# Optimization experiments

Hardware: AMD Instinct MI355X
Metric: run time of the kernel (lower is better)

Reference implementation:

```python
import jax, jax.numpy as jnp
import numpy as np

D_MODEL = 768
NUM_HEADS = 8
HEAD_DIM = D_MODEL // NUM_HEADS


def setup_inputs() -> dict:
    key = jax.random.key(0)
    ks = jax.random.split(key, 5)
    B, N = 4, 2048
    scale = 1.0 / np.sqrt(D_MODEL)
    return {
        "x": jax.random.normal(ks[0], (B, N, D_MODEL), dtype=jnp.float32),
        "W_qkv": jax.random.normal(ks[1], (D_MODEL, 3 * D_MODEL), dtype=jnp.float32) * scale,
        "b_qkv": jax.random.normal(ks[2], (3 * D_MODEL,), dtype=jnp.float32) * 0.01,
        "W_out": jax.random.normal(ks[3], (D_MODEL, D_MODEL), dtype=jnp.float32) * scale,
        "b_out": jax.random.normal(ks[4], (D_MODEL,), dtype=jnp.float32) * 0.01,
    }


def reference(x, W_qkv, b_qkv, W_out, b_out):
    B, N, _ = x.shape
    H, Dh = NUM_HEADS, HEAD_DIM
    # fused QKV projection: [B,N,3*D] -> [3,B,H,N,Dh]
    qkv = (x @ W_qkv + b_qkv).reshape(B, N, 3, H, Dh).transpose(2, 0, 3, 1, 4)
    q, k, v = qkv[0], qkv[1], qkv[2]
    # full NxN attention, as in the original (no masking)
    scores = jnp.einsum("bhnd,bhmd->bhnm", q, k) / jnp.sqrt(jnp.float32(Dh)).astype(x.dtype)
    weights = jax.nn.softmax(scores, axis=-1)
    out = jnp.einsum("bhnm,bhmd->bhnd", weights, v)  # [B,H,N,Dh]
    out = out.transpose(0, 2, 1, 3).reshape(B, N, H * Dh)
    return out @ W_out + b_out
```

## Files before the change

kernel.cpp:

```cpp
#include <hip/hip_runtime.h>
#include <hip/hip_bf16.h>
#include <math.h>

#define BB      4
#define NN      2048
#define DM      768
#define NH      8
#define DHH     96
#define BH      (BB*NH)
#define MROWS   (BB*NN)
#define NC_QKV  (3*DM)

typedef short v4s  __attribute__((ext_vector_type(4)));
typedef short v8s  __attribute__((ext_vector_type(8)));
typedef float v4f  __attribute__((ext_vector_type(4)));
typedef float v16f __attribute__((ext_vector_type(16)));
typedef unsigned int u32;

#define SCQ 0.14724599350930152f

static __device__ __forceinline__ ushort f2bf(float f) {
    __hip_bfloat16 h = __float2bfloat16(f);
    return *reinterpret_cast<ushort*>(&h);
}

static __device__ __forceinline__ void gload_lds16(const ushort* g, ushort* l) {
    __builtin_amdgcn_global_load_lds(
        (const __attribute__((address_space(1))) void*)g,
        (__attribute__((address_space(3))) void*)l, 16, 0, 0);
}

static __device__ __forceinline__ v8s load2x4_o16(const ushort* p) {
    union { v4s h[2]; v8s s; } x;
    x.h[0] = *reinterpret_cast<const v4s*>(p);
    x.h[1] = *reinterpret_cast<const v4s*>(p + 16);
    return x.s;
}

static __device__ __forceinline__ v8s pack4(u32 a, u32 b, u32 c, u32 d) {
    union { u32 u[4]; v8s s; } x;
    x.u[0] = a; x.u[1] = b; x.u[2] = c; x.u[3] = d;
    return x.s;
}
static __device__ __forceinline__ u32 bfpair(float lo, float hi) {
    return (u32)f2bf(lo) | ((u32)f2bf(hi) << 16);
}

#define CONV_NB   (MROWS * DM / 8 / 256)
#define CONVT_NB  ((DM / 32) * ((NC_QKV + DM) / 32))

__global__ __launch_bounds__(256)
void prologue_kernel(const float* __restrict__ x, ushort* __restrict__ xbf,
                     const float* __restrict__ Wq, ushort* __restrict__ Wqt,
                     const float* __restrict__ Wo, ushort* __restrict__ Wot)
{
    __shared__ ushort t[32][33];
    const int bid = blockIdx.x;

    if (bid < CONV_NB) {
        const int i = bid * 256 + threadIdx.x;
        const float4* p = reinterpret_cast<const float4*>(x) + (size_t)i * 2;
        float4 a = p[0], b = p[1];
        ushort r[8] = {f2bf(a.x), f2bf(a.y), f2bf(a.z), f2bf(a.w),
                       f2bf(b.x), f2bf(b.y), f2bf(b.z), f2bf(b.w)};
        *reinterpret_cast<v8s*>(xbf + (size_t)i * 8) = *reinterpret_cast<v8s*>(r);
        return;
    }

    const int bid2 = bid - CONV_NB;
    const int kb = bid2 % (DM / 32);
    const int nb = bid2 / (DM / 32);
    const int K = DM;
    const bool isQ = (nb < NC_QKV / 32);
    const float*  W  = isQ ? Wq  : Wo;
    ushort*       Wt = isQ ? Wqt : Wot;
    const int N  = isQ ? NC_QKV : DM;
    const int k0 = kb * 32;
    const int n0 = (isQ ? nb : nb - NC_QKV / 32) * 32;
    const int tx = threadIdx.x & 31, ty = threadIdx.x >> 5;
    #pragma unroll
    for (int r = ty; r < 32; r += 8)
        t[tx][r] = f2bf(W[(size_t)(k0 + r) * N + n0 + tx]);
    __syncthreads();
    #pragma unroll
    for (int r = ty; r < 32; r += 8)
        Wt[(size_t)(n0 + r) * K + k0 + tx] = t[r][tx];
}

template<int SCATTER>
__global__ __launch_bounds__(256)
void gemm_mfma(const ushort* __restrict__ A, const ushort* __restrict__ Bt,
               const float* __restrict__ bias, void* __restrict__ outp,
               int K, int Ncols)
{
    __shared__ ushort As[2][8192];
    __shared__ ushort Bs[2][8192];

    const int tid  = threadIdx.x;
    const int lane = tid & 63;
    const int wv   = tid >> 6;
    const int l31  = lane & 31;
    const int lhi  = lane >> 5;
    const int wr   = wv >> 1, wc = wv & 1;

    const int ny   = gridDim.y;
    const int id   = blockIdx.y * gridDim.x + blockIdx.x;
    const int c8   = id & 7;
    const int j    = id >> 3;
    const int hy   = (j >= (ny >> 1) * 8) ? 1 : 0;
    const int w    = j - hy * (ny >> 1) * 8;
    const int bx   = c8 * 8 + (w & 7);
    const int by   = hy * (ny >> 1) + (w >> 3);
    const int row0 = bx * 128;
    const int col0 = by * 128;

    v16f acc[2][2];
    #pragma unroll
    for (int mi = 0; mi < 2; ++mi)
        #pragma unroll
        for (int nj = 0; nj < 2; ++nj)
            #pragma unroll
            for (int i = 0; i < 16; ++i) acc[mi][nj][i] = 0.0f;

#define STAGE_G(bsel, kk) do {                                                  \
    _Pragma("unroll")                                                           \
    for (int c = 0; c < 4; ++c) {                                               \
        const int g   = c * 4 + wv;                                             \
        const int idx = g * 64 + lane;                                          \
        const int ss  = idx >> 7, rr = idx & 127;                               \
        gload_lds16(&A [(size_t)(row0 + rr) * K + (kk) + ss * 8],               \
                    &As[bsel][g * 512]);                                        \
        gload_lds16(&Bt[(size_t)(col0 + rr) * K + (kk) + ss * 8],               \
                    &Bs[bsel][g * 512]);                                        \
    }                                                                           \
} while (0)

    STAGE_G(0, 0);
    __syncthreads();

    const int nk = K >> 6;
    for (int t = 0; t < nk; ++t) {
        const int cur = t & 1;
        if (t + 1 < nk) STAGE_G(cur ^ 1, (t + 1) << 6);

        #pragma unroll
        for (int s16 = 0; s16 < 4; ++s16) {
            const int ks = s16 * 2 + lhi;
            v8s a0 = *reinterpret_cast<const v8s*>(&As[cur][(size_t)(ks * 128 + 64 * wr + l31) * 8]);
            v8s a1 = *reinterpret_cast<const v8s*>(&As[cur][(size_t)(ks * 128 + 64 * wr + 32 + l31) * 8]);
            v8s b0 = *reinterpret_cast<const v8s*>(&Bs[cur][(size_t)(ks * 128 + 64 * wc + l31) * 8]);
            v8s b1 = *reinterpret_cast<const v8s*>(&Bs[cur][(size_t)(ks * 128 + 64 * wc + 32 + l31) * 8]);
            acc[0][0] = __builtin_amdgcn_mfma_f32_32x32x16_bf16(a0, b0, acc[0][0], 0, 0, 0);
            acc[0][1] = __builtin_amdgcn_mfma_f32_32x32x16_bf16(a0, b1, acc[0][1], 0, 0, 0);
            acc[1][0] = __builtin_amdgcn_mfma_f32_32x32x16_bf16(a1, b0, acc[1][0], 0, 0, 0);
            acc[1][1] = __builtin_amdgcn_mfma_f32_32x32x16_bf16(a1, b1, acc[1][1], 0, 0, 0);
        }
        __syncthreads();
    }
#undef STAGE_G

    #pragma unroll
    for (int nj = 0; nj < 2; ++nj) {
        const int c = col0 + 64 * wc + 32 * nj + l31;
        const float bv = bias[c];
        #pragma unroll
        for (int mi = 0; mi < 2; ++mi) {
            #pragma unroll
            for (int r = 0; r < 16; ++r) {
                const int m = row0 + 64 * wr + 32 * mi + (r & 3) + 8 * (r >> 2) + 4 * lhi;
                float v = acc[mi][nj][r] + bv;
                if (SCATTER) {
                    const int s   = c / DM;
                    const int rem = c - s * DM;
                    const int h   = rem / DHH;
                    const int d   = rem - h * DHH;
                    const int b   = m >> 11;
                    const int n   = m & (NN - 1);
                    if (s == 0) v *= SCQ;
                    ((ushort*)outp)[((size_t)(s * BH + b * NH + h) * NN + n) * DHH + d] = f2bf(v);
                } else {
                    ((float*)outp)[(size_t)m * Ncols + c] = v;
                }
            }
        }
    }
}

__global__ __launch_bounds__(256, 2)
void attn_mfma(const ushort* __restrict__ qkv, ushort* __restrict__ attnout)
{
    __shared__ ushort Ks[6144];
    __shared__ ushort Vt[96][68];

    const int tid  = threadIdx.x;
    const int lane = tid & 63;
    const int wv   = tid >> 6;
    const int l15  = lane & 15;
    const int g4   = lane >> 4;

    const int id   = blockIdx.y * gridDim.x + blockIdx.x;
    const int c8   = id & 7;
    const int j    = id >> 3;
    const int bh   = c8 * 4 + (j & 3);
    const int qblk = j >> 2;
    const int q0   = qblk * 128;
    const int b    = bh >> 3, h = bh & 7;

    const ushort* Qg = qkv + (size_t)bh * NN * DHH;
    const ushort* Kg = qkv + ((size_t)BH + bh) * NN * DHH;
    const ushort* Vg = qkv + ((size_t)2 * BH + bh) * NN * DHH;

    v8s qf[2][3];
    #pragma unroll
    for (int qt = 0; qt < 2; ++qt)
        #pragma unroll
        for (int c = 0; c < 3; ++c)
            qf[qt][c] = *reinterpret_cast<const v8s*>(
                &Qg[(size_t)(q0 + wv * 32 + qt * 16 + l15) * DHH + c * 32 + g4 * 8]);

    v4f o[2][6];
    #pragma unroll
    for (int qt = 0; qt < 2; ++qt)
        #pragma unroll
        for (int dt = 0; dt < 6; ++dt)
            #pragma unroll
            for (int i = 0; i < 4; ++i) o[qt][dt][i] = 0.0f;
    float ds[2] = {0.0f, 0.0f};

    {
        const size_t rowb = (size_t)lane * DHH;
        v8s kr[3], vr[3];
        #pragma unroll
        for (int i = 0; i < 3; ++i) {
            kr[i] = *reinterpret_cast<const v8s*>(&Kg[rowb + (wv * 3 + i) * 8]);
            vr[i] = *reinterpret_cast<const v8s*>(&Vg[rowb + (i * 4 + wv) * 8]);
        }
        #pragma unroll
        for (int i = 0; i < 3; ++i) {
            *reinterpret_cast<v8s*>(&Ks[(wv * 3 + i) * 512 + lane * 8]) = kr[i];
            #pragma unroll
            for (int jj = 0; jj < 8; ++jj)
                Vt[(i * 4 + wv) * 8 + jj][lane] = (ushort)vr[i][jj];
        }
    }
    __syncthreads();

    for (int t = 0; t < 32; ++t) {
        v8s kr0, kr1, kr2, vr0, vr1, vr2;
        if (t < 31) {
            const size_t rowb = (size_t)((t + 1) * 64 + lane) * DHH;
            kr0 = *reinterpret_cast<const v8s*>(&Kg[rowb + (wv * 3 + 0) * 8]);
            kr1 = *reinterpret_cast<const v8s*>(&Kg[rowb + (wv * 3 + 1) * 8]);
            kr2 = *reinterpret_cast<const v8s*>(&Kg[rowb + (wv * 3 + 2) * 8]);
            vr0 = *reinterpret_cast<const v8s*>(&Vg[rowb + (0 * 4 + wv) * 8]);
            vr1 = *reinterpret_cast<const v8s*>(&Vg[rowb + (1 * 4 + wv) * 8]);
            vr2 = *reinterpret_cast<const v8s*>(&Vg[rowb + (2 * 4 + wv) * 8]);
        }

        #pragma unroll
        for (int th = 0; th < 2; ++th) {
            v4f s00, s01, s10, s11;
            #pragma unroll
            for (int i = 0; i < 4; ++i) {
                s00[i] = 0.0f; s01[i] = 0.0f; s10[i] = 0.0f; s11[i] = 0.0f;
            }
            __builtin_amdgcn_s_setprio(1);
            #pragma unroll
            for (int c = 0; c < 3; ++c) {
                v8s kf0 = *reinterpret_cast<const v8s*>(
                    &Ks[((c * 4 + g4) * 64 + (th * 2 + 0) * 16 + l15) * 8]);
                v8s kf1 = *reinterpret_cast<const v8s*>(
                    &Ks[((c * 4 + g4) * 64 + (th * 2 + 1) * 16 + l15) * 8]);
                s00 = __builtin_amdgcn_mfma_f32_16x16x32_bf16(kf0, qf[0][c], s00, 0, 0, 0);
                s01 = __builtin_amdgcn_mfma_f32_16x16x32_bf16(kf1, qf[0][c], s01, 0, 0, 0);
                s10 = __builtin_amdgcn_mfma_f32_16x16x32_bf16(kf0, qf[1][c], s10, 0, 0, 0);
                s11 = __builtin_amdgcn_mfma_f32_16x16x32_bf16(kf1, qf[1][c], s11, 0, 0, 0);
            }
            __builtin_amdgcn_s_setprio(0);

            v8s pf[2];
            #pragma unroll
            for (int qt = 0; qt < 2; ++qt) {
                const v4f& sa = qt ? s10 : s00;
                const v4f& sb = qt ? s11 : s01;
                float e0[4], e1[4];
                #pragma unroll
                for (int r = 0; r < 4; ++r) {
                    e0[r] = exp2f(sa[r]);
                    e1[r] = exp2f(sb[r]);
                    ds[qt] += e0[r] + e1[r];
                }
                pf[qt] = pack4(bfpair(e0[0], e0[1]), bfpair(e0[2], e0[3]),
                               bfpair(e1[0], e1[1]), bfpair(e1[2], e1[3]));
            }

            __builtin_amdgcn_s_setprio(1);
            #pragma unroll
            for (int dt = 0; dt < 6; ++dt) {
                const ushort* vp = &Vt[dt * 16 + l15][th * 32 + g4 * 4];
                v8s va = load2x4_o16(vp);
                o[0][dt] = __builtin_amdgcn_mfma_f32_16x16x32_bf16(va, pf[0], o[0][dt], 0, 0, 0);
                o[1][dt] = __builtin_amdgcn_mfma_f32_16x16x32_bf16(va, pf[1], o[1][dt], 0, 0, 0);
            }
            __builtin_amdgcn_s_setprio(0);
        }

        if (t < 31) {
            __syncthreads();
            *reinterpret_cast<v8s*>(&Ks[(wv * 3 + 0) * 512 + lane * 8]) = kr0;
            *reinterpret_cast<v8s*>(&Ks[(wv * 3 + 1) * 512 + lane * 8]) = kr1;
            *reinterpret_cast<v8s*>(&Ks[(wv * 3 + 2) * 512 + lane * 8]) = kr2;
            #pragma unroll
            for (int jj = 0; jj < 8; ++jj) Vt[(0 * 4 + wv) * 8 + jj][lane] = (ushort)vr0[jj];
            #pragma unroll
            for (int jj = 0; jj < 8; ++jj) Vt[(1 * 4 + wv) * 8 + jj][lane] = (ushort)vr1[jj];
            #pragma unroll
            for (int jj = 0; jj < 8; ++jj) Vt[(2 * 4 + wv) * 8 + jj][lane] = (ushort)vr2[jj];
            __syncthreads();
        }
    }

    #pragma unroll
    for (int qt = 0; qt < 2; ++qt) {
        float d = ds[qt];
        d += __shfl_xor(d, 16, 64);
        d += __shfl_xor(d, 32, 64);
        const float inv = 1.0f / d;
        const int n = q0 + wv * 32 + qt * 16 + l15;
        ushort* orow = attnout + ((size_t)(b * NN + n)) * DM + h * DHH;
        #pragma unroll
        for (int dt = 0; dt < 6; ++dt) {
            const int d0 = dt * 16 + g4 * 4;
            uint2 pk;
            pk.x = bfpair(o[qt][dt][0] * inv, o[qt][dt][1] * inv);
            pk.y = bfpair(o[qt][dt][2] * inv, o[qt][dt][3] * inv);
            *reinterpret_cast<uint2*>(&orow[d0]) = pk;
        }
    }
}

extern "C" void kernel_launch(void* const* d_in, const int* in_sizes, int n_in,
                              void* d_out, int out_size, void* d_ws, size_t ws_size,
                              hipStream_t stream)
{
    (void)in_sizes; (void)n_in; (void)out_size; (void)ws_size;
    const float* x    = (const float*)d_in[0];
    const float* Wqkv = (const float*)d_in[1];
    const float* bqkv = (const float*)d_in[2];
    const float* Wout = (const float*)d_in[3];
    const float* bout = (const float*)d_in[4];
    float* out = (float*)d_out;

    ushort* qkv   = (ushort*)d_ws;
    ushort* ao    = qkv   + (size_t)3 * BH * NN * DHH;
    ushort* xbf   = ao    + (size_t)MROWS * DM;
    ushort* wqkvt = xbf   + (size_t)MROWS * DM;
    ushort* woutt = wqkvt + (size_t)DM * NC_QKV;

    dim3 blk(256);

    prologue_kernel<<<dim3(CONV_NB + CONVT_NB), blk, 0, stream>>>(
        x, xbf, Wqkv, wqkvt, Wout, woutt);

    gemm_mfma<1><<<dim3(MROWS / 128, NC_QKV / 128), blk, 0, stream>>>(
        xbf, wqkvt, bqkv, (void*)qkv, DM, NC_QKV);

    attn_mfma<<<dim3(16, 32), blk, 0, stream>>>(qkv, ao);

    gemm_mfma<0><<<dim3(MROWS / 128, DM / 128), blk, 0, stream>>>(
        ao, woutt, bout, (void*)out, DM, DM);
}
```

Before: 200.5 us.

## Enlarge GEMM tiles to 256x256 with 8 waves and explicit vmcnt pipelining

```diff
diff --git a/kernel.cpp b/kernel.cpp
--- a/kernel.cpp
+++ b/kernel.cpp
@@ -88,35 +88,34 @@
 }
 
 template<int SCATTER>
-__global__ __launch_bounds__(256)
+__global__ __launch_bounds__(512)
 void gemm_mfma(const ushort* __restrict__ A, const ushort* __restrict__ Bt,
                const float* __restrict__ bias, void* __restrict__ outp,
                int K, int Ncols)
 {
-    __shared__ ushort As[2][8192];
-    __shared__ ushort Bs[2][8192];
+    __shared__ ushort As[2][16384];
+    __shared__ ushort Bs[2][16384];
 
     const int tid  = threadIdx.x;
     const int lane = tid & 63;
     const int wv   = tid >> 6;
     const int l31  = lane & 31;
     const int lhi  = lane >> 5;
-    const int wr   = wv >> 1, wc = wv & 1;
-
-    const int ny   = gridDim.y;
-    const int id   = blockIdx.y * gridDim.x + blockIdx.x;
-    const int c8   = id & 7;
-    const int j    = id >> 3;
-    const int hy   = (j >= (ny >> 1) * 8) ? 1 : 0;
-    const int w    = j - hy * (ny >> 1) * 8;
-    const int bx   = c8 * 8 + (w & 7);
-    const int by   = hy * (ny >> 1) + (w >> 3);
-    const int row0 = bx * 128;
-    const int col0 = by * 128;
-
-    v16f acc[2][2];
-    #pragma unroll
-    for (int mi = 0; mi < 2; ++mi)
+    const int wr   = wv >> 2;
+    const int wc   = wv & 3;
+
+    const int nwg = gridDim.x * gridDim.y;
+    const int id  = blockIdx.y * gridDim.x + blockIdx.x;
+    const int cpx = nwg >> 3;
+    const int wg  = (id & 7) * cpx + (id >> 3);
+    const int bx  = wg % gridDim.x;
+    const int by  = wg / gridDim.x;
+    const int row0 = bx * 256;
+    const int col0 = by * 256;
+
+    v16f acc[4][2];
+    #pragma unroll
+    for (int mi = 0; mi < 4; ++mi)
         #pragma unroll
         for (int nj = 0; nj < 2; ++nj)
             #pragma unroll
@@ -124,50 +123,72 @@
 
 #define STAGE_G(bsel, kk) do {                                                  \
     _Pragma("unroll")                                                           \
-    for (int c = 0; c < 4; ++c) {                                               \
-        const int g   = c * 4 + wv;                                             \
-        const int idx = g * 64 + lane;                                          \
-        const int ss  = idx >> 7, rr = idx & 127;                               \
-        gload_lds16(&A [(size_t)(row0 + rr) * K + (kk) + ss * 8],               \
-                    &As[bsel][g * 512]);                                        \
-        gload_lds16(&Bt[(size_t)(col0 + rr) * K + (kk) + ss * 8],               \
-                    &Bs[bsel][g * 512]);                                        \
+    for (int r_ = 0; r_ < 4; ++r_) {                                            \
+        const int idx_ = r_ * 512 + tid;                           \
+        const int ss_  = idx_ >> 8;                             \
+        const int rr_  = idx_ & 255;                            \
+        gload_lds16(&A [(size_t)(row0 + rr_) * K + (kk) + ss_ * 8],             \
+                    &As[bsel][(size_t)idx_ * 8]);                               \
+        gload_lds16(&Bt[(size_t)(col0 + rr_) * K + (kk) + ss_ * 8],             \
+                    &Bs[bsel][(size_t)idx_ * 8]);                               \
     }                                                                           \
 } while (0)
 
+#define FENCE() __builtin_amdgcn_sched_barrier(0)
+#define BARRIER() do { FENCE(); asm volatile("s_barrier" ::: "memory"); FENCE(); } while (0)
+
     STAGE_G(0, 0);
-    __syncthreads();
 
     const int nk = K >> 6;
     for (int t = 0; t < nk; ++t) {
         const int cur = t & 1;
-        if (t + 1 < nk) STAGE_G(cur ^ 1, (t + 1) << 6);
+
+        BARRIER();
+        if (t + 1 < nk) {
+            STAGE_G(cur ^ 1, (t + 1) << 6);
+            FENCE();
+            asm volatile("s_waitcnt vmcnt(8)" ::: "memory");
+            FENCE();
+        } else {
+            FENCE();
+            asm volatile("s_waitcnt vmcnt(0)" ::: "memory");
+            FENCE();
+        }
+        BARRIER();
 
         #pragma unroll
         for (int s16 = 0; s16 < 4; ++s16) {
             const int ks = s16 * 2 + lhi;
-            v8s a0 = *reinterpret_cast<const v8s*>(&As[cur][(size_t)(ks * 128 + 64 * wr + l31) * 8]);
-            v8s a1 = *reinterpret_cast<const v8s*>(&As[cur][(size_t)(ks * 128 + 64 * wr + 32 + l31) * 8]);
-            v8s b0 = *reinterpret_cast<const v8s*>(&Bs[cur][(size_t)(ks * 128 + 64 * wc + l31) * 8]);
-            v8s b1 = *reinterpret_cast<const v8s*>(&Bs[cur][(size_t)(ks * 128 + 64 * wc + 32 + l31) * 8]);
-            acc[0][0] = __builtin_amdgcn_mfma_f32_32x32x16_bf16(a0, b0, acc[0][0], 0, 0, 0);
-            acc[0][1] = __builtin_amdgcn_mfma_f32_32x32x16_bf16(a0, b1, acc[0][1], 0, 0, 0);
-            acc[1][0] = __builtin_amdgcn_mfma_f32_32x32x16_bf16(a1, b0, acc[1][0], 0, 0, 0);
-            acc[1][1] = __builtin_amdgcn_mfma_f32_32x32x16_bf16(a1, b1, acc[1][1], 0, 0, 0);
-        }
-        __syncthreads();
+            v8s a_[4], b_[2];
+            #pragma unroll
+            for (int mi = 0; mi < 4; ++mi)
+                a_[mi] = *reinterpret_cast<const v8s*>(
+                    &As[cur][(size_t)(ks * 256 + wr * 128 + mi * 32 + l31) * 8]);
+            #pragma unroll
+            for (int nj = 0; nj < 2; ++nj)
+                b_[nj] = *reinterpret_cast<const v8s*>(
+                    &Bs[cur][(size_t)(ks * 256 + wc * 64 + nj * 32 + l31) * 8]);
+            #pragma unroll
+            for (int mi = 0; mi < 4; ++mi)
+                #pragma unroll
+                for (int nj = 0; nj < 2; ++nj)
+                    acc[mi][nj] = __builtin_amdgcn_mfma_f32_32x32x16_bf16(
+                        a_[mi], b_[nj], acc[mi][nj], 0, 0, 0);
+        }
     }
 #undef STAGE_G
+#undef FENCE
+#undef BARRIER
 
     #pragma unroll
     for (int nj = 0; nj < 2; ++nj) {
-        const int c = col0 + 64 * wc + 32 * nj + l31;
+        const int c = col0 + wc * 64 + nj * 32 + l31;
         const float bv = bias[c];
         #pragma unroll
-        for (int mi = 0; mi < 2; ++mi) {
+        for (int mi = 0; mi < 4; ++mi) {
             #pragma unroll
             for (int r = 0; r < 16; ++r) {
-                const int m = row0 + 64 * wr + 32 * mi + (r & 3) + 8 * (r >> 2) + 4 * lhi;
+                const int m = row0 + wr * 128 + mi * 32 + (r & 3) + 8 * (r >> 2) + 4 * lhi;
                 float v = acc[mi][nj][r] + bv;
                 if (SCATTER) {
                     const int s   = c / DM;
@@ -357,16 +378,14 @@
     ushort* wqkvt = xbf   + (size_t)MROWS * DM;
     ushort* woutt = wqkvt + (size_t)DM * NC_QKV;
 
-    dim3 blk(256);
-
-    prologue_kernel<<<dim3(CONV_NB + CONVT_NB), blk, 0, stream>>>(
+    prologue_kernel<<<dim3(CONV_NB + CONVT_NB), dim3(256), 0, stream>>>(
         x, xbf, Wqkv, wqkvt, Wout, woutt);
 
-    gemm_mfma<1><<<dim3(MROWS / 128, NC_QKV / 128), blk, 0, stream>>>(
+    gemm_mfma<1><<<dim3(MROWS / 256, NC_QKV / 256), dim3(512), 0, stream>>>(
         xbf, wqkvt, bqkv, (void*)qkv, DM, NC_QKV);
 
-    attn_mfma<<<dim3(16, 32), blk, 0, stream>>>(qkv, ao);
-
-    gemm_mfma<0><<<dim3(MROWS / 128, DM / 128), blk, 0, stream>>>(
+    attn_mfma<<<dim3(16, 32), dim3(256), 0, stream>>>(qkv, ao);
+
+    gemm_mfma<0><<<dim3(MROWS / 256, DM / 256), dim3(512), 0, stream>>>(
         ao, woutt, bout, (void*)out, DM, DM);
 }
```

New measurement: 241.6 us. +20.5%, slower.
